# Optimization experiments

Measured on AMD Instinct MI355X. Metric: run time of the kernel, lower is better.

Reference implementation:

```python
import jax, jax.numpy as jnp
import numpy as np

B, N = 4, 65536
Z_DIM, HIDDEN, N_LAYERS = 64, 128, 4
PE_FREQS = 10
FEAT_RES = 16  # global_feat_res
IN_DIM = Z_DIM + 3 + 3 * 2 * PE_FREQS  # latent + pos-encoded coords


def setup_inputs() -> dict:
    key = jax.random.key(0)
    ks = jax.random.split(key, 4 + 2 * N_LAYERS)
    inp = {}
    # xyz in [-1,1]: used directly as grid_sample grid coordinates
    inp['xyz'] = jax.random.uniform(ks[0], (B, N, 3), jnp.float32, -1.0, 1.0)
    inp['local_latents'] = jax.random.normal(ks[1], (B, Z_DIM, FEAT_RES, FEAT_RES), jnp.float32)
    dims = [IN_DIM] + [HIDDEN] * N_LAYERS
    for i in range(N_LAYERS):
        inp[f'W{i}'] = jax.random.normal(ks[2 + i], (dims[i], dims[i + 1]), jnp.float32) / np.sqrt(dims[i]).astype(np.float32)
        inp[f'b{i}'] = jnp.zeros((dims[i + 1],), jnp.float32)
    inp['Wa'] = jax.random.normal(ks[2 + N_LAYERS], (HIDDEN, 1), jnp.float32) / np.sqrt(HIDDEN).astype(np.float32)
    inp['ba'] = jnp.zeros((1,), jnp.float32)
    return inp


def grid_sample_2d(img, grid):
    # torch F.grid_sample: bilinear, align_corners=False, padding_mode='zeros'
    # img [B,C,H,W], grid [B,Hg,Wg,2] in [-1,1], (x,y) order -> out [B,C,Hg,Wg]
    _, _, H, W = img.shape
    x = (grid[..., 0] + 1.0) * (W * 0.5) - 0.5
    y = (grid[..., 1] + 1.0) * (H * 0.5) - 0.5
    x0 = jnp.floor(x); y0 = jnp.floor(y)
    x1 = x0 + 1.0; y1 = y0 + 1.0

    def gather(ix, iy):
        valid = (ix >= 0) & (ix <= W - 1) & (iy >= 0) & (iy <= H - 1)
        ixc = jnp.clip(ix, 0, W - 1).astype(jnp.int32)
        iyc = jnp.clip(iy, 0, H - 1).astype(jnp.int32)
        v = jax.vmap(lambda im, yy, xx: im[:, yy, xx])(img, iyc, ixc)  # [B,C,Hg,Wg]
        return v * valid[:, None].astype(img.dtype)

    out = (gather(x0, y0) * ((x1 - x) * (y1 - y))[:, None]
           + gather(x0, y1) * ((x1 - x) * (y - y0))[:, None]
           + gather(x1, y0) * ((x - x0) * (y1 - y))[:, None]
           + gather(x1, y1) * ((x - x0) * (y - y0))[:, None])
    return out


def positional_encoding(x):
    # x [P,3] -> [P, 3 + 3*2*PE_FREQS]
    freqs = 2.0 ** jnp.arange(PE_FREQS, dtype=x.dtype)
    ang = x[..., None, :] * freqs[:, None]  # [P, L, 3]
    P = x.shape[0]
    return jnp.concatenate([x, jnp.sin(ang).reshape(P, -1), jnp.cos(ang).reshape(P, -1)], axis=-1)


def _forward(xyz, local_latents, Ws, bs, Wa, ba):
    xyz4 = xyz[:, None]  # [B, 1, N, 3] (forward's xyz.unsqueeze(1))
    # sample_local_latents: 4D latents -> grid = xyz[..., [0, 2]]
    grid = jnp.stack([xyz4[..., 0], xyz4[..., 2]], axis=-1)  # [B,1,N,2]
    samp = grid_sample_2d(local_latents, grid)               # [B,C,1,N]
    z = samp.transpose(0, 2, 3, 1).reshape(-1, Z_DIM)        # [B*N, C]
    # get_local_coordinates (preserve_y=True since latents are 4D)
    lc = (xyz4 + 1.0) * 0.5 * FEAT_RES
    lc = lc - jnp.round(lc - 0.5)  # round-half-to-even matches torch .round()
    lc = lc * 2.0 - 1.0
    coords = jnp.concatenate([lc[..., 0:1], xyz4[..., 1:2], lc[..., 2:3]], axis=-1).reshape(-1, 3)
    # local_generator MLP (viewdirs=None on alpha-only path)
    h = jnp.concatenate([z, positional_encoding(coords)], axis=-1)
    for W, b in zip(Ws, bs):
        h = jax.nn.relu(h @ W + b)
    alpha = h @ Wa + ba  # [B*N, 1], raw alpha (activation happens in volume render, not here)
    return alpha.reshape(xyz.shape[0], 1, -1)  # alpha.view(B, n_samples=1, samples_per_ray=N)


def reference(xyz, local_latents, W0, b0, W1, b1, W2, b2, W3, b3, Wa, ba):
    return _forward(xyz, local_latents, (W0, W1, W2, W3), (b0, b1, b2, b3), Wa, ba)
```

## Files before the change

kernel.cpp:

```cpp
#include <hip/hip_runtime.h>
#include <hip/hip_bf16.h>

typedef float f32x4 __attribute__((ext_vector_type(4)));
typedef short bf16x8 __attribute__((ext_vector_type(8)));
typedef const __attribute__((address_space(1))) unsigned gas_u32;
typedef __attribute__((address_space(3))) unsigned las_u32;

__device__ __forceinline__ unsigned pk2(float lo, float hi) {
  union { __hip_bfloat162 h2; unsigned u; } c;
  c.h2 = __float22bfloat162_rn(make_float2(lo, hi));
  return c.u;
}
__device__ __forceinline__ ushort f2bf1(float f) {
  union { __hip_bfloat16 h; ushort u; } c;
  c.h = __float2bfloat16(f);
  return c.u;
}
__device__ __forceinline__ float u2f(unsigned u) {
  union { unsigned u; float f; } c; c.u = u; return c.f;
}

__global__ void pack_all(const float* __restrict__ W0, const float* __restrict__ W1,
                         const float* __restrict__ W2, const float* __restrict__ W3,
                         const float* __restrict__ b0, const float* __restrict__ b1,
                         const float* __restrict__ b2, const float* __restrict__ b3,
                         const float* __restrict__ lat,
                         ushort* __restrict__ wpk, float* __restrict__ biasf,
                         ushort* __restrict__ latpk) {
  int t = blockIdx.x * 256 + threadIdx.x;
  if (t < 8192) {
    int lane = t & 63, kt = (t >> 6) & 3, jt = (t >> 8) & 7, layer = t >> 11;
    const float* W = layer == 0 ? W0 : layer == 1 ? W1 : layer == 2 ? W2 : W3;
    int K = (layer == 0) ? 127 : 128;
    int g = lane >> 4, r = lane & 15;
    bf16x8 pk;
#pragma unroll
    for (int i = 0; i < 8; i++) {
      int k = kt * 32 + 8 * g + i;
      pk[i] = (short)((k < K) ? f2bf1(W[k * 128 + jt * 16 + r]) : (ushort)0);
    }
    *(bf16x8*)(wpk + ((t >> 11) * 32 + (jt * 4 + kt)) * 512 + lane * 8) = pk;
  } else if (t < 16384) {
    int t2 = t - 8192;
    int g = t2 & 7, pix = (t2 >> 3) & 255, b = t2 >> 11;
    uint4 w;
    unsigned* wp = &w.x;
#pragma unroll
    for (int i = 0; i < 4; i++)
      wp[i] = pk2(lat[(b * 64 + 8 * g + 2 * i) * 256 + pix],
                  lat[(b * 64 + 8 * g + 2 * i + 1) * 256 + pix]);
    *(uint4*)((char*)latpk + b * 32768 + pix * 128 + ((16 * g) ^ ((pix & 7) << 4))) = w;
  } else if (t < 16896) {
    int t3 = t - 16384;
    int layer = t3 >> 7, j = t3 & 127;
    const float* b = layer == 0 ? b0 : layer == 1 ? b1 : layer == 2 ? b2 : b3;
    biasf[t3] = b[j];
  }
}

__global__ __launch_bounds__(256, 4) void scene_fwd(
    const float* __restrict__ xyz, const ushort* __restrict__ latpk,
    const ushort* __restrict__ wpk, const float* __restrict__ biasf,
    const float* __restrict__ wa, const float* __restrict__ ba,
    float* __restrict__ out) {
  __shared__ char smem[32768];
  const int tid = threadIdx.x;
  const int wave = tid >> 6, lane = tid & 63;
  const int g = lane >> 4, r = lane & 15;
  const int p0 = blockIdx.x * 128;
  const int batch = blockIdx.x >> 9;

  const int t2 = tid & 127;
  const int p = p0 + t2;
  const float X = xyz[3 * p + 0], Y = xyz[3 * p + 1], Z = xyz[3 * p + 2];

  {
    const char* src = (const char*)latpk + batch * 32768;
#pragma unroll
    for (int i = 0; i < 8; i++) {
      const int off = (wave * 8 + i) * 1024;
      __builtin_amdgcn_global_load_lds((gas_u32*)(src + off + lane * 16),
                                       (las_u32*)(smem + off), 16, 0, 0);
    }
  }
  __syncthreads();

  uint4 fr[8];
  if (tid < 128) {
    float gx = (X + 1.f) * 8.f - 0.5f;
    float gy = (Z + 1.f) * 8.f - 0.5f;
    float x0f = floorf(gx), y0f = floorf(gy);
    float fx = gx - x0f, fy = gy - y0f;
    int ix0 = (int)x0f, iy0 = (int)y0f;
    int ix1 = ix0 + 1, iy1 = iy0 + 1;
    float vx0 = (ix0 >= 0 && ix0 <= 15) ? 1.f : 0.f;
    float vx1 = (ix1 >= 0 && ix1 <= 15) ? 1.f : 0.f;
    float vy0 = (iy0 >= 0 && iy0 <= 15) ? 1.f : 0.f;
    float vy1 = (iy1 >= 0 && iy1 <= 15) ? 1.f : 0.f;
    int cx0 = min(max(ix0, 0), 15), cx1 = min(max(ix1, 0), 15);
    int cy0 = min(max(iy0, 0), 15), cy1 = min(max(iy1, 0), 15);
    float w00 = (1.f - fx) * (1.f - fy) * vx0 * vy0;
    float w01 = (1.f - fx) * fy * vx0 * vy1;
    float w10 = fx * (1.f - fy) * vx1 * vy0;
    float w11 = fx * fy * vx1 * vy1;
    int px00 = cy0 * 16 + cx0, px01 = cy1 * 16 + cx0;
    int px10 = cy0 * 16 + cx1, px11 = cy1 * 16 + cx1;
    int o00 = px00 * 128, s00 = (px00 & 7) << 4;
    int o01 = px01 * 128, s01 = (px01 & 7) << 4;
    int o10 = px10 * 128, s10 = (px10 & 7) << 4;
    int o11 = px11 * 128, s11 = (px11 & 7) << 4;
#pragma unroll
    for (int gr = 0; gr < 8; gr++) {
      const int off = 16 * gr;
      float f[8];
#pragma unroll
      for (int i = 0; i < 8; i++) f[i] = 0.f;
#pragma unroll
      for (int c = 0; c < 4; c++) {
        const char* ap = smem + (c == 0 ? o00 + (off ^ s00) : c == 1 ? o01 + (off ^ s01)
                               : c == 2 ? o10 + (off ^ s10) : o11 + (off ^ s11));
        const float wc = c == 0 ? w00 : c == 1 ? w01 : c == 2 ? w10 : w11;
        uint4 cv = *(const uint4*)ap;
        const unsigned* u = &cv.x;
#pragma unroll
        for (int q = 0; q < 4; q++) {
          f[2 * q]     += wc * u2f(u[q] << 16);
          f[2 * q + 1] += wc * u2f(u[q] & 0xffff0000u);
        }
      }
      fr[gr].x = pk2(f[0], f[1]); fr[gr].y = pk2(f[2], f[3]);
      fr[gr].z = pk2(f[4], f[5]); fr[gr].w = pk2(f[6], f[7]);
    }
  } else {
    float lcx = (X + 1.f) * 8.f; lcx = lcx - rintf(lcx - 0.5f); lcx = lcx * 2.f - 1.f;
    float lcz = (Z + 1.f) * 8.f; lcz = lcz - rintf(lcz - 0.5f); lcz = lcz * 2.f - 1.f;
    const float c0 = lcx, c1 = Y, c2 = lcz;
#pragma unroll
    for (int gr = 0; gr < 8; gr++) {
      unsigned* wo = &fr[gr].x;
#pragma unroll
      for (int q = 0; q < 4; q++) {
        float e[2];
#pragma unroll
        for (int h = 0; h < 2; h++) {
          const int idx = 8 * gr + 2 * q + h;
          float v;
          if (idx == 0) v = c0;
          else if (idx == 1) v = c1;
          else if (idx == 2) v = c2;
          else if (idx == 63) v = 0.f;
          else if (idx < 33) {
            const int s = idx - 3;
            const int d = s % 3;
            const float cc = d == 0 ? c0 : d == 1 ? c1 : c2;
            v = __sinf(cc * (float)(1 << (s / 3)));
          } else {
            const int s = idx - 33;
            const int d = s % 3;
            const float cc = d == 0 ? c0 : d == 1 ? c1 : c2;
            v = __cosf(cc * (float)(1 << (s / 3)));
          }
          e[h] = v;
        }
        wo[q] = pk2(e[0], e[1]);
      }
    }
  }
  __syncthreads();

  {
    const int tile = t2 >> 6, row = t2 & 63;
    char* rowp = smem + tile * 16384 + row * 256;
    const unsigned swz = (unsigned)((row & 7) << 4);
    const int base = (tid < 128) ? 0 : 128;
#pragma unroll
    for (int gr = 0; gr < 8; gr++)
      *(uint4*)(rowp + (((unsigned)(base + 16 * gr)) ^ swz)) = fr[gr];
  }
  __syncthreads();

  const int tileM = wave >> 1;
  const int jh = wave & 1;
  char* hb = smem + tileM * 16384;
  f32x4 acc[4][4];
#pragma unroll 1
  for (int layer = 0; layer < 4; layer++) {
    const float* bias = biasf + layer * 128;
    const ushort* Aw = wpk + layer * 16384;
#pragma unroll
    for (int jt = 0; jt < 4; jt++) {
      f32x4 bf = *(const f32x4*)(bias + (jh * 4 + jt) * 16 + 4 * g);
#pragma unroll
      for (int pt = 0; pt < 4; pt++) acc[jt][pt] = bf;
    }
#pragma unroll
    for (int kt = 0; kt < 4; kt++) {
      bf16x8 Bf[4];
#pragma unroll
      for (int pt = 0; pt < 4; pt++) {
        const int pr = pt * 16 + r;
        Bf[pt] = *(const bf16x8*)(hb + pr * 256 +
                  (((unsigned)(kt * 64 + 16 * g)) ^ ((unsigned)((pr & 7) << 4))));
      }
      __builtin_amdgcn_s_setprio(1);
#pragma unroll
      for (int jt = 0; jt < 4; jt++) {
        bf16x8 Af = *(const bf16x8*)(Aw + ((jh * 4 + jt) * 4 + kt) * 512 + lane * 8);
#pragma unroll
        for (int pt = 0; pt < 4; pt++)
          acc[jt][pt] = __builtin_amdgcn_mfma_f32_16x16x32_bf16(Af, Bf[pt], acc[jt][pt], 0, 0, 0);
      }
      __builtin_amdgcn_s_setprio(0);
    }
    if (layer < 3) {
      __syncthreads();
#pragma unroll
      for (int jt = 0; jt < 4; jt++) {
#pragma unroll
        for (int pt = 0; pt < 4; pt++) {
          const int pr = pt * 16 + r;
          uint2 w;
          w.x = pk2(fmaxf(acc[jt][pt][0], 0.f), fmaxf(acc[jt][pt][1], 0.f));
          w.y = pk2(fmaxf(acc[jt][pt][2], 0.f), fmaxf(acc[jt][pt][3], 0.f));
          *(uint2*)(hb + pr * 256 +
                    (((unsigned)(32 * (jh * 4 + jt) + 8 * g)) ^ ((unsigned)((pr & 7) << 4)))) = w;
        }
      }
      __syncthreads();
    }
  }

  const float ba0 = ba[0];
  float part[4] = {0.f, 0.f, 0.f, 0.f};
#pragma unroll
  for (int jt = 0; jt < 4; jt++) {
    f32x4 wf = *(const f32x4*)(wa + (jh * 4 + jt) * 16 + 4 * g);
#pragma unroll
    for (int pt = 0; pt < 4; pt++) {
#pragma unroll
      for (int i = 0; i < 4; i++)
        part[pt] += fmaxf(acc[jt][pt][i], 0.f) * wf[i];
    }
  }
  __syncthreads();
  float* scr = (float*)smem;
#pragma unroll
  for (int pt = 0; pt < 4; pt++) {
    float s = part[pt];
    s += __shfl_xor(s, 16, 64);
    s += __shfl_xor(s, 32, 64);
    if (lane < 16) scr[(tileM * 2 + jh) * 64 + pt * 16 + lane] = s;
  }
  __syncthreads();
  if (jh == 0 && lane < 16) {
#pragma unroll
    for (int pt = 0; pt < 4; pt++) {
      const int idx = pt * 16 + lane;
      out[p0 + tileM * 64 + idx] =
          scr[(tileM * 2) * 64 + idx] + scr[(tileM * 2 + 1) * 64 + idx] + ba0;
    }
  }
}

extern "C" void kernel_launch(void* const* d_in, const int* in_sizes, int n_in,
                              void* d_out, int out_size, void* d_ws, size_t ws_size,
                              hipStream_t stream) {
  const float* xyz = (const float*)d_in[0];
  const float* lat = (const float*)d_in[1];
  const float* W0 = (const float*)d_in[2];
  const float* b0 = (const float*)d_in[3];
  const float* W1 = (const float*)d_in[4];
  const float* b1 = (const float*)d_in[5];
  const float* W2 = (const float*)d_in[6];
  const float* b2 = (const float*)d_in[7];
  const float* W3 = (const float*)d_in[8];
  const float* b3 = (const float*)d_in[9];
  const float* wa = (const float*)d_in[10];
  const float* ba = (const float*)d_in[11];
  float* out = (float*)d_out;
  ushort* wpk = (ushort*)d_ws;
  float* biasf = (float*)((char*)d_ws + 131072);
  ushort* latpk = (ushort*)((char*)d_ws + 139264);

  pack_all<<<66, 256, 0, stream>>>(W0, W1, W2, W3, b0, b1, b2, b3, lat,
                                   wpk, biasf, latpk);
  scene_fwd<<<2048, 256, 0, stream>>>(xyz, latpk, wpk, biasf, wa, ba, out);
}
```

Measured before the change: 52.65 us.

## Keep latent grid in fp32 in LDS and double block size to 512 threads

The packed latent grid is now stored as fp32 rather than bf16, so bilinear sampling reads float4 values directly with no bf16 unpacking. The block grows to 512 threads covering 256 points, and LDS doubles to 64KB to hold the fp32 latent tile per batch. This cuts the ALU work in the sampling stage. In exchange it doubles LDS traffic for the latent load and reduces how many blocks fit per CU. The MLP stage's tile/wave mapping appears unchanged in the visible code, while the hidden region may depend on wave indices that now go up to 8.

```diff
diff --git a/kernel.cpp b/kernel.cpp
--- a/kernel.cpp
+++ b/kernel.cpp
@@ -15,9 +15,6 @@
   union { __hip_bfloat16 h; ushort u; } c;
   c.h = __float2bfloat16(f);
   return c.u;
-}
-__device__ __forceinline__ float u2f(unsigned u) {
-  union { unsigned u; float f; } c; c.u = u; return c.f;
 }
 
 __global__ void pack_all(const float* __restrict__ W0, const float* __restrict__ W1,
@@ -26,7 +23,7 @@
                          const float* __restrict__ b2, const float* __restrict__ b3,
                          const float* __restrict__ lat,
                          ushort* __restrict__ wpk, float* __restrict__ biasf,
-                         ushort* __restrict__ latpk) {
+                         float* __restrict__ latf) {
   int t = blockIdx.x * 256 + threadIdx.x;
   if (t < 8192) {
     int lane = t & 63, kt = (t >> 6) & 3, jt = (t >> 8) & 7, layer = t >> 11;
@@ -40,45 +37,42 @@
       pk[i] = (short)((k < K) ? f2bf1(W[k * 128 + jt * 16 + r]) : (ushort)0);
     }
     *(bf16x8*)(wpk + ((t >> 11) * 32 + (jt * 4 + kt)) * 512 + lane * 8) = pk;
-  } else if (t < 16384) {
+  } else if (t < 8192 + 16384) {
     int t2 = t - 8192;
-    int g = t2 & 7, pix = (t2 >> 3) & 255, b = t2 >> 11;
-    uint4 w;
-    unsigned* wp = &w.x;
-#pragma unroll
-    for (int i = 0; i < 4; i++)
-      wp[i] = pk2(lat[(b * 64 + 8 * g + 2 * i) * 256 + pix],
-                  lat[(b * 64 + 8 * g + 2 * i + 1) * 256 + pix]);
-    *(uint4*)((char*)latpk + b * 32768 + pix * 128 + ((16 * g) ^ ((pix & 7) << 4))) = w;
-  } else if (t < 16896) {
-    int t3 = t - 16384;
+    int q = t2 & 15, pix = (t2 >> 4) & 255, b = t2 >> 12;
+    f32x4 v;
+#pragma unroll
+    for (int i = 0; i < 4; i++) v[i] = lat[(b * 64 + 4 * q + i) * 256 + pix];
+    *(f32x4*)((char*)latf + b * 65536 + pix * 256 + ((16 * q) ^ ((pix & 7) << 4))) = v;
+  } else if (t < 8192 + 16384 + 512) {
+    int t3 = t - (8192 + 16384);
     int layer = t3 >> 7, j = t3 & 127;
     const float* b = layer == 0 ? b0 : layer == 1 ? b1 : layer == 2 ? b2 : b3;
     biasf[t3] = b[j];
   }
 }
 
-__global__ __launch_bounds__(256, 4) void scene_fwd(
-    const float* __restrict__ xyz, const ushort* __restrict__ latpk,
+__global__ __launch_bounds__(512, 4) void scene_fwd(
+    const float* __restrict__ xyz, const float* __restrict__ latf,
     const ushort* __restrict__ wpk, const float* __restrict__ biasf,
     const float* __restrict__ wa, const float* __restrict__ ba,
     float* __restrict__ out) {
-  __shared__ char smem[32768];
+  __shared__ char smem[65536];
   const int tid = threadIdx.x;
   const int wave = tid >> 6, lane = tid & 63;
   const int g = lane >> 4, r = lane & 15;
-  const int p0 = blockIdx.x * 128;
-  const int batch = blockIdx.x >> 9;
-
-  const int t2 = tid & 127;
+  const int p0 = blockIdx.x * 256;
+  const int batch = blockIdx.x >> 8;
+
+  const int t2 = tid & 255;
   const int p = p0 + t2;
   const float X = xyz[3 * p + 0], Y = xyz[3 * p + 1], Z = xyz[3 * p + 2];
 
   {
-    const char* src = (const char*)latpk + batch * 32768;
+    const char* src = (const char*)latf + batch * 65536;
 #pragma unroll
     for (int i = 0; i < 8; i++) {
-      const int off = (wave * 8 + i) * 1024;
+      const int off = (i * 8 + wave) * 1024;
       __builtin_amdgcn_global_load_lds((gas_u32*)(src + off + lane * 16),
                                        (las_u32*)(smem + off), 16, 0, 0);
     }
@@ -86,7 +80,7 @@
   __syncthreads();
 
   uint4 fr[8];
-  if (tid < 128) {
+  if (tid < 256) {
     float gx = (X + 1.f) * 8.f - 0.5f;
     float gy = (Z + 1.f) * 8.f - 0.5f;
     float x0f = floorf(gx), y0f = floorf(gy);
@@ -105,28 +99,23 @@
     float w11 = fx * fy * vx1 * vy1;
     int px00 = cy0 * 16 + cx0, px01 = cy1 * 16 + cx0;
     int px10 = cy0 * 16 + cx1, px11 = cy1 * 16 + cx1;
-    int o00 = px00 * 128, s00 = (px00 & 7) << 4;
-    int o01 = px01 * 128, s01 = (px01 & 7) << 4;
-    int o10 = px10 * 128, s10 = (px10 & 7) << 4;
-    int o11 = px11 * 128, s11 = (px11 & 7) << 4;
+    int o00 = px00 * 256, s00 = (px00 & 7) << 4;
+    int o01 = px01 * 256, s01 = (px01 & 7) << 4;
+    int o10 = px10 * 256, s10 = (px10 & 7) << 4;
+    int o11 = px11 * 256, s11 = (px11 & 7) << 4;
 #pragma unroll
     for (int gr = 0; gr < 8; gr++) {
-      const int off = 16 * gr;
       float f[8];
 #pragma unroll
-      for (int i = 0; i < 8; i++) f[i] = 0.f;
-#pragma unroll
-      for (int c = 0; c < 4; c++) {
-        const char* ap = smem + (c == 0 ? o00 + (off ^ s00) : c == 1 ? o01 + (off ^ s01)
-                               : c == 2 ? o10 + (off ^ s10) : o11 + (off ^ s11));
-        const float wc = c == 0 ? w00 : c == 1 ? w01 : c == 2 ? w10 : w11;
-        uint4 cv = *(const uint4*)ap;
-        const unsigned* u = &cv.x;
-#pragma unroll
-        for (int q = 0; q < 4; q++) {
-          f[2 * q]     += wc * u2f(u[q] << 16);
-          f[2 * q + 1] += wc * u2f(u[q] & 0xffff0000u);
-        }
+      for (int u = 0; u < 2; u++) {
+        const int off = 32 * gr + 16 * u;
+        f32x4 c00 = *(const f32x4*)(smem + o00 + (off ^ s00));
+        f32x4 c01 = *(const f32x4*)(smem + o01 + (off ^ s01));
+        f32x4 c10 = *(const f32x4*)(smem + o10 + (off ^ s10));
+        f32x4 c11 = *(const f32x4*)(smem + o11 + (off ^ s11));
+#pragma unroll
+        for (int i = 0; i < 4; i++)
+          f[4 * u + i] = w00 * c00[i] + w01 * c01[i] + w10 * c10[i] + w11 * c11[i];
       }
       fr[gr].x = pk2(f[0], f[1]); fr[gr].y = pk2(f[2], f[3]);
       fr[gr].z = pk2(f[4], f[5]); fr[gr].w = pk2(f[6], f[7]);
@@ -172,7 +161,7 @@
     const int tile = t2 >> 6, row = t2 & 63;
     char* rowp = smem + tile * 16384 + row * 256;
     const unsigned swz = (unsigned)((row & 7) << 4);
-    const int base = (tid < 128) ? 0 : 128;
+    const int base = (tid < 256) ? 0 : 128;
 #pragma unroll
     for (int gr = 0; gr < 8; gr++)
       *(uint4*)(rowp + (((unsigned)(base + 16 * gr)) ^ swz)) = fr[gr];
@@ -280,9 +269,9 @@
   float* out = (float*)d_out;
   ushort* wpk = (ushort*)d_ws;
   float* biasf = (float*)((char*)d_ws + 131072);
-  ushort* latpk = (ushort*)((char*)d_ws + 139264);
-
-  pack_all<<<66, 256, 0, stream>>>(W0, W1, W2, W3, b0, b1, b2, b3, lat,
-                                   wpk, biasf, latpk);
-  scene_fwd<<<2048, 256, 0, stream>>>(xyz, latpk, wpk, biasf, wa, ba, out);
-}
+  float* latf = (float*)((char*)d_ws + 139264);
+
+  pack_all<<<98, 256, 0, stream>>>(W0, W1, W2, W3, b0, b1, b2, b3, lat,
+                                   wpk, biasf, latf);
+  scene_fwd<<<1024, 512, 0, stream>>>(xyz, latf, wpk, biasf, wa, ba, out);
+}
```

After: 53.35 us. About the same (+1.3%).

## Switch MLP layers to 32x32x16 bf16 MFMA with repacked weight layout

Applied to the files above, without the earlier changes.

Replaces the 16x16x32 MFMA tiling (4x4 accumulators per wave) with 32x32x16 MFMA (2x2 f32x16 accumulators) and repacks the weights to match the new operand layout. The larger tiles mean fewer weight and activation fragment loads per flop and fewer MFMA issues. The epilogue writeback, bias init and final reduction are reworked for the 32-row layout. The bilinear gather accumulation is also rewritten with float2 vectors so the compiler can use packed FMA.

```diff
diff --git a/kernel.cpp b/kernel.cpp
--- a/kernel.cpp
+++ b/kernel.cpp
@@ -2,6 +2,8 @@
 #include <hip/hip_bf16.h>
 
 typedef float f32x4 __attribute__((ext_vector_type(4)));
+typedef float f32x2 __attribute__((ext_vector_type(2)));
+typedef float f32x16 __attribute__((ext_vector_type(16)));
 typedef short bf16x8 __attribute__((ext_vector_type(8)));
 typedef const __attribute__((address_space(1))) unsigned gas_u32;
 typedef __attribute__((address_space(3))) unsigned las_u32;
@@ -29,17 +31,17 @@
                          ushort* __restrict__ latpk) {
   int t = blockIdx.x * 256 + threadIdx.x;
   if (t < 8192) {
-    int lane = t & 63, kt = (t >> 6) & 3, jt = (t >> 8) & 7, layer = t >> 11;
+    int lane = t & 63, ks = (t >> 6) & 7, jtg = (t >> 9) & 3, layer = t >> 11;
     const float* W = layer == 0 ? W0 : layer == 1 ? W1 : layer == 2 ? W2 : W3;
     int K = (layer == 0) ? 127 : 128;
-    int g = lane >> 4, r = lane & 15;
+    int j = 32 * jtg + (lane & 31);
     bf16x8 pk;
 #pragma unroll
     for (int i = 0; i < 8; i++) {
-      int k = kt * 32 + 8 * g + i;
-      pk[i] = (short)((k < K) ? f2bf1(W[k * 128 + jt * 16 + r]) : (ushort)0);
-    }
-    *(bf16x8*)(wpk + ((t >> 11) * 32 + (jt * 4 + kt)) * 512 + lane * 8) = pk;
+      int k = 16 * ks + 8 * (lane >> 5) + i;
+      pk[i] = (short)((k < K) ? f2bf1(W[k * 128 + j]) : (ushort)0);
+    }
+    *(bf16x8*)(wpk + t * 8) = pk;
   } else if (t < 16384) {
     int t2 = t - 8192;
     int g = t2 & 7, pix = (t2 >> 3) & 255, b = t2 >> 11;
@@ -66,7 +68,6 @@
   __shared__ char smem[32768];
   const int tid = threadIdx.x;
   const int wave = tid >> 6, lane = tid & 63;
-  const int g = lane >> 4, r = lane & 15;
   const int p0 = blockIdx.x * 128;
   const int batch = blockIdx.x >> 9;
 
@@ -112,9 +113,9 @@
 #pragma unroll
     for (int gr = 0; gr < 8; gr++) {
       const int off = 16 * gr;
-      float f[8];
-#pragma unroll
-      for (int i = 0; i < 8; i++) f[i] = 0.f;
+      f32x2 f2[4];
+#pragma unroll
+      for (int q = 0; q < 4; q++) f2[q] = (f32x2){0.f, 0.f};
 #pragma unroll
       for (int c = 0; c < 4; c++) {
         const char* ap = smem + (c == 0 ? o00 + (off ^ s00) : c == 1 ? o01 + (off ^ s01)
@@ -124,12 +125,12 @@
         const unsigned* u = &cv.x;
 #pragma unroll
         for (int q = 0; q < 4; q++) {
-          f[2 * q]     += wc * u2f(u[q] << 16);
-          f[2 * q + 1] += wc * u2f(u[q] & 0xffff0000u);
+          f32x2 cw = {u2f(u[q] << 16), u2f(u[q] & 0xffff0000u)};
+          f2[q] += cw * wc;
         }
       }
-      fr[gr].x = pk2(f[0], f[1]); fr[gr].y = pk2(f[2], f[3]);
-      fr[gr].z = pk2(f[4], f[5]); fr[gr].w = pk2(f[6], f[7]);
+      fr[gr].x = pk2(f2[0][0], f2[0][1]); fr[gr].y = pk2(f2[1][0], f2[1][1]);
+      fr[gr].z = pk2(f2[2][0], f2[2][1]); fr[gr].w = pk2(f2[3][0], f2[3][1]);
     }
   } else {
     float lcx = (X + 1.f) * 8.f; lcx = lcx - rintf(lcx - 0.5f); lcx = lcx * 2.f - 1.f;
@@ -182,48 +183,62 @@
   const int tileM = wave >> 1;
   const int jh = wave & 1;
   char* hb = smem + tileM * 16384;
-  f32x4 acc[4][4];
+  const int col = lane & 31;
+  const int kh = lane >> 5;
+  f32x16 acc[2][2];
 #pragma unroll 1
   for (int layer = 0; layer < 4; layer++) {
     const float* bias = biasf + layer * 128;
     const ushort* Aw = wpk + layer * 16384;
 #pragma unroll
-    for (int jt = 0; jt < 4; jt++) {
-      f32x4 bf = *(const f32x4*)(bias + (jh * 4 + jt) * 16 + 4 * g);
-#pragma unroll
-      for (int pt = 0; pt < 4; pt++) acc[jt][pt] = bf;
-    }
-#pragma unroll
-    for (int kt = 0; kt < 4; kt++) {
-      bf16x8 Bf[4];
-#pragma unroll
-      for (int pt = 0; pt < 4; pt++) {
-        const int pr = pt * 16 + r;
+    for (int jt = 0; jt < 2; jt++) {
+#pragma unroll
+      for (int q = 0; q < 4; q++) {
+        f32x4 bv = *(const f32x4*)(bias + (2 * jh + jt) * 32 + 8 * q + 4 * kh);
+#pragma unroll
+        for (int c = 0; c < 4; c++) {
+          acc[jt][0][4 * q + c] = bv[c];
+          acc[jt][1][4 * q + c] = bv[c];
+        }
+      }
+    }
+#pragma unroll
+    for (int ks = 0; ks < 8; ks++) {
+      bf16x8 Bf[2];
+#pragma unroll
+      for (int pt = 0; pt < 2; pt++) {
+        const int pr = pt * 32 + col;
         Bf[pt] = *(const bf16x8*)(hb + pr * 256 +
-                  (((unsigned)(kt * 64 + 16 * g)) ^ ((unsigned)((pr & 7) << 4))));
+                  (((unsigned)(32 * ks + 16 * kh)) ^ ((unsigned)((pr & 7) << 4))));
       }
       __builtin_amdgcn_s_setprio(1);
 #pragma unroll
-      for (int jt = 0; jt < 4; jt++) {
-        bf16x8 Af = *(const bf16x8*)(Aw + ((jh * 4 + jt) * 4 + kt) * 512 + lane * 8);
-#pragma unroll
-        for (int pt = 0; pt < 4; pt++)
-          acc[jt][pt] = __builtin_amdgcn_mfma_f32_16x16x32_bf16(Af, Bf[pt], acc[jt][pt], 0, 0, 0);
+      for (int jt = 0; jt < 2; jt++) {
+        bf16x8 Af = *(const bf16x8*)(Aw + (2 * jh + jt) * 4096 + ks * 512 + lane * 8);
+#pragma unroll
+        for (int pt = 0; pt < 2; pt++)
+          acc[jt][pt] = __builtin_amdgcn_mfma_f32_32x32x16_bf16(Af, Bf[pt], acc[jt][pt], 0, 0, 0);
       }
       __builtin_amdgcn_s_setprio(0);
     }
     if (layer < 3) {
       __syncthreads();
 #pragma unroll
-      for (int jt = 0; jt < 4; jt++) {
-#pragma unroll
-        for (int pt = 0; pt < 4; pt++) {
-          const int pr = pt * 16 + r;
-          uint2 w;
-          w.x = pk2(fmaxf(acc[jt][pt][0], 0.f), fmaxf(acc[jt][pt][1], 0.f));
-          w.y = pk2(fmaxf(acc[jt][pt][2], 0.f), fmaxf(acc[jt][pt][3], 0.f));
-          *(uint2*)(hb + pr * 256 +
-                    (((unsigned)(32 * (jh * 4 + jt) + 8 * g)) ^ ((unsigned)((pr & 7) << 4)))) = w;
+      for (int jt = 0; jt < 2; jt++) {
+#pragma unroll
+        for (int pt = 0; pt < 2; pt++) {
+          const int pr = pt * 32 + col;
+          const unsigned swz = (unsigned)((pr & 7) << 4);
+#pragma unroll
+          for (int q = 0; q < 4; q++) {
+            uint2 w;
+            w.x = pk2(fmaxf(acc[jt][pt][4 * q + 0], 0.f),
+                      fmaxf(acc[jt][pt][4 * q + 1], 0.f));
+            w.y = pk2(fmaxf(acc[jt][pt][4 * q + 2], 0.f),
+                      fmaxf(acc[jt][pt][4 * q + 3], 0.f));
+            *(uint2*)(hb + pr * 256 +
+                      (((unsigned)((2 * jh + jt) * 64 + 16 * q + 8 * kh)) ^ swz)) = w;
+          }
         }
       }
       __syncthreads();
@@ -231,34 +246,32 @@
   }
 
   const float ba0 = ba[0];
-  float part[4] = {0.f, 0.f, 0.f, 0.f};
-#pragma unroll
-  for (int jt = 0; jt < 4; jt++) {
-    f32x4 wf = *(const f32x4*)(wa + (jh * 4 + jt) * 16 + 4 * g);
-#pragma unroll
-    for (int pt = 0; pt < 4; pt++) {
-#pragma unroll
-      for (int i = 0; i < 4; i++)
-        part[pt] += fmaxf(acc[jt][pt][i], 0.f) * wf[i];
+  float part[2] = {0.f, 0.f};
+#pragma unroll
+  for (int jt = 0; jt < 2; jt++) {
+#pragma unroll
+    for (int q = 0; q < 4; q++) {
+      f32x4 wf = *(const f32x4*)(wa + (2 * jh + jt) * 32 + 8 * q + 4 * kh);
+#pragma unroll
+      for (int pt = 0; pt < 2; pt++) {
+#pragma unroll
+        for (int c = 0; c < 4; c++)
+          part[pt] += fmaxf(acc[jt][pt][4 * q + c], 0.f) * wf[c];
+      }
     }
   }
   __syncthreads();
   float* scr = (float*)smem;
 #pragma unroll
-  for (int pt = 0; pt < 4; pt++) {
+  for (int pt = 0; pt < 2; pt++) {
     float s = part[pt];
-    s += __shfl_xor(s, 16, 64);
     s += __shfl_xor(s, 32, 64);
-    if (lane < 16) scr[(tileM * 2 + jh) * 64 + pt * 16 + lane] = s;
-  }
-  __syncthreads();
-  if (jh == 0 && lane < 16) {
-#pragma unroll
-    for (int pt = 0; pt < 4; pt++) {
-      const int idx = pt * 16 + lane;
-      out[p0 + tileM * 64 + idx] =
-          scr[(tileM * 2) * 64 + idx] + scr[(tileM * 2 + 1) * 64 + idx] + ba0;
-    }
+    if (lane < 32) scr[(tileM * 2 + jh) * 64 + pt * 32 + lane] = s;
+  }
+  __syncthreads();
+  if (tid < 128) {
+    const int tile = tid >> 6, loc = tid & 63;
+    out[p0 + tid] = scr[(tile * 2) * 64 + loc] + scr[(tile * 2 + 1) * 64 + loc] + ba0;
   }
 }
 
```

Measured after the change: 55.46 us. 5.3% more time.
